# Kernel optimization log

Hardware: AMD Instinct MI355X
Metric: run time of the kernel (lower is better)

Reference implementation:

```python
import jax, jax.numpy as jnp
import numpy as np

T = 2048          # tokens (single causal sequence)
HID = 4096        # hidden_size
H = 32            # num_heads
DQ = 256          # per-head q/k dim (192 nope + 64 rope)
DN = 192          # nope dim
DR = 64           # rope dim
DV = 256          # v head dim
DKV = 512         # kv latent rank
QLORA = 2048      # q lora rank
EPS = 1e-6
THETA = 10000.0
SCALE = DQ ** -0.5


def rmsnorm(x, w):
    return x * jax.lax.rsqrt(jnp.mean(x * x, axis=-1, keepdims=True) + EPS) * w


def rope_neox(pos, x):
    # x: [T, h, DR]; neox style: rotate concatenated halves
    inv_freq = 1.0 / (THETA ** (jnp.arange(0, DR, 2, dtype=jnp.float32) / DR))  # [DR/2]
    ang = pos.astype(jnp.float32)[:, None] * inv_freq  # [T, DR/2]
    cos = jnp.cos(ang)[:, None, :]
    sin = jnp.sin(ang)[:, None, :]
    x1, x2 = jnp.split(x, 2, axis=-1)
    return jnp.concatenate([x1 * cos - x2 * sin, x2 * cos + x1 * sin], axis=-1)


def setup_inputs() -> dict:
    key = jax.random.key(0)
    ks = jax.random.split(key, 8)
    s = 0.02
    return {
        "hidden_states": jax.random.normal(ks[0], (T, HID), dtype=jnp.float32),
        "positions": jnp.arange(T, dtype=jnp.int32),
        "wq_a": jax.random.normal(ks[1], (HID, QLORA), dtype=jnp.float32) * s,
        "q_a_ln_w": jnp.ones((QLORA,), dtype=jnp.float32),
        "wq_b": jax.random.normal(ks[2], (QLORA, H * DQ), dtype=jnp.float32) * s,
        "wkv_a": jax.random.normal(ks[3], (HID, DKV + DR), dtype=jnp.float32) * s,
        "kv_a_ln_w": jnp.ones((DKV,), dtype=jnp.float32),
        "wkv_b": jax.random.normal(ks[4], (DKV, H * (DN + DV)), dtype=jnp.float32) * s,
        "wo": jax.random.normal(ks[5], (H * DV, HID), dtype=jnp.float32) * s,
    }


def reference(hidden_states, positions, wq_a, q_a_ln_w, wq_b, wkv_a, kv_a_ln_w, wkv_b, wo):
    # q path: lora down -> rmsnorm -> up -> [T, H, 256]
    q = rmsnorm(hidden_states @ wq_a, q_a_ln_w)
    q = (q @ wq_b).reshape(T, H, DQ)
    # kv path: latent 512 + shared k_pe 64
    latent = hidden_states @ wkv_a
    kv_a, k_pe = jnp.split(latent, [DKV], axis=-1)
    kv_a = rmsnorm(kv_a, kv_a_ln_w)
    kv = (kv_a @ wkv_b).reshape(T, H, DN + DV)
    k_nope, v = jnp.split(kv, [DN], axis=-1)
    q_nope, q_pe = jnp.split(q, [DN], axis=-1)
    k_pe = k_pe.reshape(T, 1, DR)
    q_pe = rope_neox(positions, q_pe)
    k_pe = rope_neox(positions, k_pe)
    q = jnp.concatenate([q_nope, q_pe], axis=-1)                       # [T, H, 256]
    k = jnp.concatenate([k_nope, jnp.broadcast_to(k_pe, (T, H, DR))], axis=-1)
    # causal attention
    scores = jnp.einsum("thd,shd->hts", q, k) * SCALE                  # [H, T, T]
    causal = jnp.tril(jnp.ones((T, T), dtype=bool))
    scores = jnp.where(causal[None], scores, jnp.finfo(scores.dtype).min)
    attn = jax.nn.softmax(scores, axis=-1)
    out = jnp.einsum("hts,shd->thd", attn, v).reshape(T, H * DV)
    return out @ wo
```

## Files before the change

### kernel.cpp

```cpp
#include <hip/hip_runtime.h>
#include <cstdint>
#include <cstddef>

#define T_    2048
#define HID_  4096
#define NH_   32
#define DQ_   256
#define DN_   192
#define DR_   64
#define DV_   256
#define DKV_  512
#define QL_   2048
#define NKV_  576
#define NKVP_ 640
#define HDQ_  8192
#define HDKV_ 14336
#define HDV_  8192
#define SCALE_ 0.0625f
#define MN5_  8388608
#define SK5_  2
#define MN1_  4194304
#define SK1_  4

using bf16x8 = __attribute__((ext_vector_type(8))) short;
using f32x4  = __attribute__((ext_vector_type(4))) float;

__device__ ushort g_hb   [(size_t)T_*HID_];
__device__ ushort g_wtqa [(size_t)QL_*HID_];
__device__ ushort g_wtqb [(size_t)HDQ_*QL_];
__device__ ushort g_wtkva[(size_t)NKVP_*HID_];
__device__ ushort g_wtkvb[(size_t)HDKV_*DKV_];
__device__ ushort g_wto  [(size_t)HID_*HDV_];
__device__ float  g_qa   [(size_t)T_*QL_];
__device__ ushort g_qn   [(size_t)T_*QL_];
__device__ ushort g_q    [(size_t)T_*HDQ_];
__device__ float  g_lat  [(size_t)T_*NKVP_];
__device__ ushort g_kvn  [(size_t)T_*DKV_];
__device__ ushort g_kpe  [(size_t)T_*DR_];
__device__ ushort g_kv   [(size_t)T_*HDKV_];
__device__ ushort g_k    [(size_t)NH_*T_*DQ_];
__device__ ushort g_vt   [(size_t)NH_*DV_*T_];
__device__ ushort g_o    [(size_t)T_*HDV_];
__device__ float  g_p5   [(size_t)SK5_*MN5_];

__device__ __forceinline__ float b2f(ushort h){ union{unsigned u; float f;} x; x.u=((unsigned)h)<<16; return x.f; }
__device__ __forceinline__ ushort f2b(float f){ union{float f; unsigned u;} x; x.f=f; unsigned r=x.u + 0x7fffu + ((x.u>>16)&1u); return (ushort)(r>>16); }
__device__ __forceinline__ void storeC(float*  p, float v){ *p = v; }
__device__ __forceinline__ void storeC(ushort* p, float v){ *p = f2b(v); }

#define GLD16(gp, lp) __builtin_amdgcn_global_load_lds( \
    (const __attribute__((address_space(1))) unsigned*)(gp), \
    (__attribute__((address_space(3))) unsigned*)(lp), 16, 0, 0)

__global__ __launch_bounds__(256) void convert_hidden(const float* __restrict__ src) {
  size_t i = ((size_t)blockIdx.x*256 + threadIdx.x)*4;
  float4 v = *(const float4*)(src + i);
  ushort4 o; o.x=f2b(v.x); o.y=f2b(v.y); o.z=f2b(v.z); o.w=f2b(v.w);
  *(ushort4*)(g_hb + i) = o;
}

__global__ __launch_bounds__(256) void transpose_w(const float* __restrict__ W,
                                                   ushort* __restrict__ Wt,
                                                   int K, int N, int Npad) {
  __shared__ float tile[64][33];
  const int bk = blockIdx.x*64, bn = blockIdx.y*32;
  const int tx = threadIdx.x & 31, ty = threadIdx.x >> 5;
  for (int r = ty; r < 64; r += 8) {
    int n = bn + tx;
    tile[r][tx] = (n < N) ? W[(size_t)(bk + r)*N + n] : 0.f;
  }
  __syncthreads();
  for (int rr = ty; rr < 32; rr += 8) {
    int n = bn + rr;
    unsigned pv = (unsigned)f2b(tile[2*tx][rr]) | ((unsigned)f2b(tile[2*tx+1][rr]) << 16);
    ((unsigned*)(Wt + (size_t)n*K))[(bk>>1) + tx] = pv;
  }
}

template<typename OutT>
__global__ __launch_bounds__(256) void gemm_bt(const ushort* __restrict__ A,
                                               const ushort* __restrict__ Bt,
                                               OutT* __restrict__ C,
                                               int M, int N, int K) {
  __shared__ ushort As[128*32];
  __shared__ ushort Bs[128*32];
  const int tid = threadIdx.x, lane = tid & 63, w = tid >> 6;
  const int wr = w >> 1, wc = w & 1, l15 = lane & 15, l4 = lane >> 4;
  const int m0 = blockIdx.x*128, n0 = blockIdx.y*128;
  f32x4 acc[4][4];
  #pragma unroll
  for (int i=0;i<4;i++)
    #pragma unroll
    for (int j=0;j<4;j++) acc[i][j] = f32x4{0.f,0.f,0.f,0.f};

  const int le0 = tid*8, le1 = (256+tid)*8;
  const int r0 = le0>>5, c0 = le0&31, r1 = le1>>5, c1 = le1&31;
  for (int k0 = 0; k0 < K; k0 += 32) {
    GLD16(A  + (size_t)(m0 + r0)*K + k0 + c0, ((ushort*)As)+le0);
    GLD16(A  + (size_t)(m0 + r1)*K + k0 + c1, ((ushort*)As)+le1);
    GLD16(Bt + (size_t)(n0 + r0)*K + k0 + c0, ((ushort*)Bs)+le0);
    GLD16(Bt + (size_t)(n0 + r1)*K + k0 + c1, ((ushort*)Bs)+le1);
    __syncthreads();
    bf16x8 af[4], bfr[4];
    #pragma unroll
    for (int i=0;i<4;i++) af[i]  = *(const bf16x8*)(As + (wr*64 + i*16 + l15)*32 + 8*l4);
    #pragma unroll
    for (int j=0;j<4;j++) bfr[j] = *(const bf16x8*)(Bs + (wc*64 + j*16 + l15)*32 + 8*l4);
    #pragma unroll
    for (int i=0;i<4;i++)
      #pragma unroll
      for (int j=0;j<4;j++)
        acc[i][j] = __builtin_amdgcn_mfma_f32_16x16x32_bf16(af[i], bfr[j], acc[i][j], 0,0,0);
    __syncthreads();
  }
  #pragma unroll
  for (int i=0;i<4;i++)
    #pragma unroll
    for (int j=0;j<4;j++) {
      const int row = m0 + wr*64 + i*16 + l4*4;
      const int col = n0 + wc*64 + j*16 + l15;
      #pragma unroll
      for (int r=0;r<4;r++) storeC(&C[(size_t)(row+r)*N + col], acc[i][j][r]);
    }
}

template<typename OutT, int S>
__global__ __launch_bounds__(512, 2) void gemm8(const ushort* __restrict__ A,
                                                const ushort* __restrict__ Bt,
                                                OutT* __restrict__ C,
                                                int M, int N, int Kfull, int pstride) {
  __shared__ ushort sm[65536];
  const int tid = threadIdx.x, lane = tid & 63, w = tid >> 6;
  const int wr = w >> 2, wc = w & 3, l15 = lane & 15, l4 = lane >> 4;
  const int swm = (l15 & 7) << 3;
  const int gm = M >> 8, gn = N >> 8;
  const int nb = gridDim.x, id = blockIdx.x;
  const int swz = (id & 7) * (nb >> 3) + (id >> 3);
  const int m0 = (swz % gm) << 8;
  const int rest = swz / gm;
  const int n0 = (rest % gn) << 8;
  const int ks = rest / gn;
  const int Ksl = Kfull / S;
  const int kofs = ks * Ksl;
  const int NT = Ksl >> 6;

#define STG_A(tt, qm) do { const int p_=(tt)&1, kb_=kofs+(tt)*64; \
    _Pragma("unroll") \
    for (int i_=0;i_<2;i_++){ \
      const int le_=(i_*512+tid)*8, r_=le_>>6, c_=le_&63; \
      const int tr_=(r_>>6)*128 + (qm)*64 + (r_&63); \
      GLD16(A + (size_t)(m0+tr_)*Kfull + kb_ + (c_ ^ ((r_&7)<<3)), \
            sm + p_*16384 + (qm)*8192 + le_); } } while(0)
#define STG_B(tt, qn) do { const int p_=(tt)&1, kb_=kofs+(tt)*64; \
    _Pragma("unroll") \
    for (int i_=0;i_<2;i_++){ \
      const int le_=(i_*512+tid)*8, r_=le_>>6, c_=le_&63; \
      const int tr_=(r_>>5)*64 + (qn)*32 + (r_&31); \
      GLD16(Bt + (size_t)(n0+tr_)*Kfull + kb_ + (c_ ^ ((r_&7)<<3)), \
            sm + 32768 + p_*16384 + (qn)*8192 + le_); } } while(0)

  f32x4 acc[8][4];
  #pragma unroll
  for (int i=0;i<8;i++)
    #pragma unroll
    for (int j=0;j<4;j++) acc[i][j] = f32x4{0.f,0.f,0.f,0.f};

  STG_A(0,0); STG_B(0,0); STG_A(0,1); STG_B(0,1);
  if (NT > 1) { STG_A(1,0); STG_B(1,0); }
  __builtin_amdgcn_sched_barrier(0);
  if (NT > 1) asm volatile("s_waitcnt vmcnt(4)" ::: "memory");
  else        asm volatile("s_waitcnt vmcnt(0)" ::: "memory");
  __builtin_amdgcn_sched_barrier(0);
  __builtin_amdgcn_s_barrier();

  for (int t = 0; t < NT; ++t) {
    const int p = t & 1;
    const ushort* Ab = sm + p*16384;
    const ushort* Bb = sm + 32768 + p*16384;
    bf16x8 af[4][2], bq0[2][2], bq1[2][2];

    #pragma unroll
    for (int mi=0;mi<4;mi++)
      #pragma unroll
      for (int k2=0;k2<2;k2++)
        af[mi][k2] = *(const bf16x8*)(Ab + (wr*64 + mi*16 + l15)*64 + ((k2*32 + 8*l4) ^ swm));
    #pragma unroll
    for (int nf=0;nf<2;nf++)
      #pragma unroll
      for (int k2=0;k2<2;k2++)
        bq0[nf][k2] = *(const bf16x8*)(Bb + (wc*32 + nf*16 + l15)*64 + ((k2*32 + 8*l4) ^ swm));
    if (t + 1 < NT) STG_A(t+1, 1);
    __builtin_amdgcn_sched_barrier(0);
    __builtin_amdgcn_s_barrier();
    __builtin_amdgcn_s_setprio(1);
    #pragma unroll
    for (int mi=0;mi<4;mi++)
      #pragma unroll
      for (int nf=0;nf<2;nf++)
        #pragma unroll
        for (int k2=0;k2<2;k2++)
          acc[mi][nf] = __builtin_amdgcn_mfma_f32_16x16x32_bf16(af[mi][k2], bq0[nf][k2], acc[mi][nf], 0,0,0);
    __builtin_amdgcn_s_setprio(0);
    __builtin_amdgcn_sched_barrier(0);
    __builtin_amdgcn_s_barrier();

    #pragma unroll
    for (int nf=0;nf<2;nf++)
      #pragma unroll
      for (int k2=0;k2<2;k2++)
        bq1[nf][k2] = *(const bf16x8*)(Bb + 8192 + (wc*32 + nf*16 + l15)*64 + ((k2*32 + 8*l4) ^ swm));
    if (t + 1 < NT) STG_B(t+1, 1);
    __builtin_amdgcn_sched_barrier(0);
    __builtin_amdgcn_s_barrier();
    __builtin_amdgcn_s_setprio(1);
    #pragma unroll
    for (int mi=0;mi<4;mi++)
      #pragma unroll
      for (int nf=0;nf<2;nf++)
        #pragma unroll
        for (int k2=0;k2<2;k2++)
          acc[mi][2+nf] = __builtin_amdgcn_mfma_f32_16x16x32_bf16(af[mi][k2], bq1[nf][k2], acc[mi][2+nf], 0,0,0);
    __builtin_amdgcn_s_setprio(0);
    __builtin_amdgcn_sched_barrier(0);
    __builtin_amdgcn_s_barrier();

    #pragma unroll
    for (int mi=0;mi<4;mi++)
      #pragma unroll
      for (int k2=0;k2<2;k2++)
        af[mi][k2] = *(const bf16x8*)(Ab + 8192 + (wr*64 + mi*16 + l15)*64 + ((k2*32 + 8*l4) ^ swm));
    if (t + 2 < NT) STG_A(t+2, 0);
    __builtin_amdgcn_sched_barrier(0);
    __builtin_amdgcn_s_barrier();
    __builtin_amdgcn_s_setprio(1);
    #pragma unroll
    for (int mi=0;mi<4;mi++)
      #pragma unroll
      for (int nf=0;nf<2;nf++)
        #pragma unroll
        for (int k2=0;k2<2;k2++)
          acc[4+mi][nf] = __builtin_amdgcn_mfma_f32_16x16x32_bf16(af[mi][k2], bq0[nf][k2], acc[4+mi][nf], 0,0,0);
    __builtin_amdgcn_s_setprio(0);
    __builtin_amdgcn_sched_barrier(0);
    __builtin_amdgcn_s_barrier();

    if (t + 2 < NT) STG_B(t+2, 0);
    __builtin_amdgcn_sched_barrier(0);
    if (t + 2 < NT)      asm volatile("s_waitcnt vmcnt(4)" ::: "memory");
    else if (t + 1 < NT) asm volatile("s_waitcnt vmcnt(0)" ::: "memory");
    __builtin_amdgcn_sched_barrier(0);
    __builtin_amdgcn_s_barrier();
    __builtin_amdgcn_s_setprio(1);
    #pragma unroll
    for (int mi=0;mi<4;mi++)
      #pragma unroll
      for (int nf=0;nf<2;nf++)
        #pragma unroll
        for (int k2=0;k2<2;k2++)
          acc[4+mi][2+nf] = __builtin_amdgcn_mfma_f32_16x16x32_bf16(af[mi][k2], bq1[nf][k2], acc[4+mi][2+nf], 0,0,0);
    __builtin_amdgcn_s_setprio(0);
    __builtin_amdgcn_sched_barrier(0);
    __builtin_amdgcn_s_barrier();
  }
#undef STG_A
#undef STG_B
  asm volatile("s_waitcnt vmcnt(0)" ::: "memory");

  #pragma unroll
  for (int mi=0;mi<8;mi++)
    #pragma unroll
    for (int nj=0;nj<4;nj++) {
      const int row = m0 + wr*128 + mi*16 + l4*4;
      const int col = n0 + wc*64 + nj*16 + l15;
      #pragma unroll
      for (int r=0;r<4;r++) {
        if (S == 1) storeC(&C[(size_t)(row+r)*N + col], acc[mi][nj][r]);
        else ((float*)C)[(size_t)ks*pstride + (size_t)(row+r)*N + col] = acc[mi][nj][r];
      }
    }
}

__global__ __launch_bounds__(256) void reduce5(const float* __restrict__ p, float* __restrict__ out) {
  size_t i = ((size_t)blockIdx.x*256 + threadIdx.x)*4;
  float4 a = *(const float4*)(p + i);
  #pragma unroll
  for (int s=1; s<SK5_; s++) {
    float4 b = *(const float4*)(p + (size_t)s*MN5_ + i);
    a.x+=b.x; a.y+=b.y; a.z+=b.z; a.w+=b.w;
  }
  *(float4*)(out + i) = a;
}

__global__ __launch_bounds__(256) void rmsnorm_q(const float* __restrict__ p,
                                                 const float* __restrict__ wln) {
  const int row = blockIdx.x;
  const float* x = p + (size_t)row*QL_;
  float* xo = g_qa + (size_t)row*QL_;
  float ss = 0.f;
  for (int i = threadIdx.x; i < QL_/4; i += 256) {
    float4 v = ((const float4*)x)[i];
    #pragma unroll
    for (int s=1; s<SK1_; s++) {
      float4 b = *(const float4*)(x + (size_t)s*MN1_ + i*4);
      v.x+=b.x; v.y+=b.y; v.z+=b.z; v.w+=b.w;
    }
    ((float4*)xo)[i] = v;
    ss += v.x*v.x + v.y*v.y + v.z*v.z + v.w*v.w;
  }
  #pragma unroll
  for (int o=32;o>=1;o>>=1) ss += __shfl_xor(ss, o);
  __shared__ float sr[4];
  if ((threadIdx.x & 63) == 0) sr[threadIdx.x>>6] = ss;
  __syncthreads();
  float rs = rsqrtf((sr[0]+sr[1]+sr[2]+sr[3])/(float)QL_ + 1e-6f);
  for (int i = threadIdx.x; i < QL_; i += 256)
    g_qn[(size_t)row*QL_ + i] = f2b(xo[i]*rs*wln[i]);
}

__global__ __launch_bounds__(256) void kv_norm_rope(const float* __restrict__ wln,
                                                    const int* __restrict__ pos) {
  const int t = blockIdx.x;
  const float* lat = g_lat + (size_t)t*NKVP_;
  float ss = 0.f;
  for (int i = threadIdx.x; i < DKV_; i += 256) ss += lat[i]*lat[i];
  #pragma unroll
  for (int o=32;o>=1;o>>=1) ss += __shfl_xor(ss, o);
  __shared__ float sr[4];
  if ((threadIdx.x & 63) == 0) sr[threadIdx.x>>6] = ss;
  __syncthreads();
  float rs = rsqrtf((sr[0]+sr[1]+sr[2]+sr[3])/(float)DKV_ + 1e-6f);
  for (int i = threadIdx.x; i < DKV_; i += 256)
    g_kvn[(size_t)t*DKV_ + i] = f2b(lat[i]*rs*wln[i]);
  if (threadIdx.x < 32) {
    const int i = threadIdx.x;
    float p = (float)pos[t];
    float ang = p * powf(10000.f, -(float)i/32.f);
    float c = cosf(ang), s = sinf(ang);
    float x1 = lat[DKV_ + i], x2 = lat[DKV_ + 32 + i];
    g_kpe[(size_t)t*DR_ + i]      = f2b(x1*c - x2*s);
    g_kpe[(size_t)t*DR_ + 32 + i] = f2b(x2*c + x1*s);
  }
}

__global__ __launch_bounds__(256) void q_rope(const int* __restrict__ pos) {
  const int t = blockIdx.x;
  __shared__ float cs[32], sn[32];
  if (threadIdx.x < 32) {
    const int i = threadIdx.x;
    float p = (float)pos[t];
    float ang = p * powf(10000.f, -(float)i/32.f);
    cs[i] = cosf(ang); sn[i] = sinf(ang);
  }
  __syncthreads();
  for (int e = threadIdx.x; e < NH_*32; e += 256) {
    const int h = e >> 5, i = e & 31;
    ushort* qp = g_q + (size_t)t*HDQ_ + h*DQ_ + DN_;
    float x1 = b2f(qp[i]), x2 = b2f(qp[32 + i]);
    qp[i]      = f2b(x1*cs[i] - x2*sn[i]);
    qp[32 + i] = f2b(x2*cs[i] + x1*sn[i]);
  }
}

__global__ __launch_bounds__(256) void build_k() {
  const int t = blockIdx.x;
  for (int e = threadIdx.x; e < NH_*32; e += 256) {
    const int h = e >> 5, d = (e & 31)*8;
    uint4 v;
    if (d < DN_) v = *(const uint4*)(g_kv  + (size_t)t*HDKV_ + h*448 + d);
    else         v = *(const uint4*)(g_kpe + (size_t)t*DR_ + (d - DN_));
    *(uint4*)(g_k + ((size_t)h*T_ + t)*DQ_ + d) = v;
  }
}

__global__ __launch_bounds__(256) void build_vt() {
  const int h = blockIdx.x, tt = blockIdx.y;
  __shared__ ushort tile[64*272];
  const int tid = threadIdx.x;
  #pragma unroll
  for (int p=0;p<8;p++) {
    int le = (p*256+tid)*8;
    int tl = le >> 8, d = le & 255;
    uint4 v = *(const uint4*)(g_kv + (size_t)(tt*64 + tl)*HDKV_ + h*448 + DN_ + d);
    *(uint4*)(tile + tl*272 + d) = v;
  }
  __syncthreads();
  #pragma unroll
  for (int p=0;p<8;p++) {
    int le = (p*256+tid)*8;
    int d = le >> 6, tl0 = le & 63;
    ushort tmp[8];
    #pragma unroll
    for (int j=0;j<8;j++) tmp[j] = tile[(tl0+j)*272 + d];
    *(uint4*)(g_vt + ((size_t)h*DV_ + d)*T_ + tt*64 + tl0) = *(const uint4*)tmp;
  }
}

__global__ __launch_bounds__(256) void attn_kernel() {
  __shared__ ushort KV[64*256];
  __shared__ ushort Pl[4][16][64];
  const int h = blockIdx.x;
  const int qt = (gridDim.y - 1) - blockIdx.y;
  const int tid = threadIdx.x, lane = tid & 63, w = tid >> 6;
  const int l15 = lane & 15, l4 = lane >> 4;
  const int swm = (l15 & 7) << 3;

  const ushort* Kh = g_k  + (size_t)h*T_*DQ_;
  const ushort* Vh = g_vt + (size_t)h*DV_*T_;

#define STAGE_K(kt_) do { \
    const ushort* ks_ = Kh + (size_t)(kt_)*64*DQ_; \
    _Pragma("unroll") \
    for (int c_=0;c_<8;c_++){ int le_=(c_*256+tid)*8, r_=le_>>8, co_=le_&255; \
      GLD16(ks_ + r_*256 + (co_ ^ ((r_&7)<<3)), KV+le_); } } while(0)
#define STAGE_V(kt_) do { \
    _Pragma("unroll") \
    for (int c_=0;c_<8;c_++){ int le_=(c_*256+tid)*8, d_=le_>>6, kv_=le_&63; \
      GLD16(Vh + (size_t)d_*T_ + (kt_)*64 + (kv_ ^ ((d_&7)<<3)), KV+le_); } } while(0)

  const int q0 = qt*64;
  const int qrow = q0 + w*16 + l15;

  bf16x8 qf[8];
  {
    const ushort* qb = g_q + (size_t)qrow*HDQ_ + h*DQ_;
    #pragma unroll
    for (int g=0; g<8; g++) qf[g] = *(const bf16x8*)(qb + 32*g + 8*l4);
  }
  f32x4 acc[16];
  #pragma unroll
  for (int i=0;i<16;i++) acc[i] = f32x4{0.f,0.f,0.f,0.f};
  float m_r = -1e30f, l_r = 0.f;

  STAGE_K(0);

  for (int kt = 0; kt <= qt; ++kt) {
    __builtin_amdgcn_sched_barrier(0);
    asm volatile("s_waitcnt vmcnt(0)" ::: "memory");
    __builtin_amdgcn_sched_barrier(0);
    __builtin_amdgcn_s_barrier();

    f32x4 s[4];
    #pragma unroll
    for (int fn=0; fn<4; fn++) s[fn] = f32x4{0.f,0.f,0.f,0.f};
    __builtin_amdgcn_s_setprio(1);
    #pragma unroll
    for (int g=0; g<8; g++)
      #pragma unroll
      for (int fn=0; fn<4; fn++) {
        bf16x8 kf = *(const bf16x8*)(KV + (fn*16 + l15)*256 + ((32*g + 8*l4) ^ swm));
        s[fn] = __builtin_amdgcn_mfma_f32_16x16x32_bf16(kf, qf[g], s[fn], 0,0,0);
      }
    __builtin_amdgcn_s_setprio(0);
    asm volatile("s_waitcnt lgkmcnt(0)" ::: "memory");
    __builtin_amdgcn_sched_barrier(0);
    __builtin_amdgcn_s_barrier();
    STAGE_V(kt);
    __builtin_amdgcn_sched_barrier(0);

    if (kt == qt) {
      #pragma unroll
      for (int fn=0; fn<4; fn++)
        #pragma unroll
        for (int r=0;r<4;r++) {
          int kv = kt*64 + fn*16 + l4*4 + r;
          if (kv > qrow) s[fn][r] = -1e30f;
        }
    }

    float mx = s[0][0];
    #pragma unroll
    for (int fn=0; fn<4; fn++)
      #pragma unroll
      for (int r=0;r<4;r++) mx = fmaxf(mx, s[fn][r]);
    mx = fmaxf(mx, __shfl_xor(mx, 16));
    mx = fmaxf(mx, __shfl_xor(mx, 32));
    mx *= SCALE_;
    if (__any(mx > m_r)) {
      float mn = fmaxf(m_r, mx);
      float sc = __expf(m_r - mn);
      m_r = mn;
      l_r *= sc;
      #pragma unroll
      for (int fd=0; fd<16; fd++)
        #pragma unroll
        for (int r=0;r<4;r++) acc[fd][r] *= sc;
    }
    float ssum = 0.f;
    #pragma unroll
    for (int fn=0; fn<4; fn++)
      #pragma unroll
      for (int r=0;r<4;r++) {
        float p = __expf(fmaf(s[fn][r], SCALE_, -m_r));
        s[fn][r] = p; ssum += p;
      }
    ssum += __shfl_xor(ssum, 16);
    ssum += __shfl_xor(ssum, 32);
    l_r += ssum;

    #pragma unroll
    for (int fn=0; fn<4; fn++) {
      ushort4 pw;
      pw.x = f2b(s[fn][0]); pw.y = f2b(s[fn][1]);
      pw.z = f2b(s[fn][2]); pw.w = f2b(s[fn][3]);
      *(ushort4*)(&Pl[w][l15][(fn*16 + l4*4) ^ swm]) = pw;
    }

    __builtin_amdgcn_sched_barrier(0);
    asm volatile("s_waitcnt vmcnt(0)" ::: "memory");
    __builtin_amdgcn_sched_barrier(0);
    __builtin_amdgcn_s_barrier();

    __builtin_amdgcn_s_setprio(1);
    #pragma unroll
    for (int s2=0; s2<2; s2++) {
      bf16x8 pa = *(const bf16x8*)(&Pl[w][l15][(s2*32 + 8*l4) ^ swm]);
      #pragma unroll
      for (int fd=0; fd<16; fd++) {
        bf16x8 vb = *(const bf16x8*)(KV + (fd*16 + l15)*64 + ((s2*32 + 8*l4) ^ swm));
        acc[fd] = __builtin_amdgcn_mfma_f32_16x16x32_bf16(vb, pa, acc[fd], 0,0,0);
      }
    }
    __builtin_amdgcn_s_setprio(0);
    asm volatile("s_waitcnt lgkmcnt(0)" ::: "memory");
    __builtin_amdgcn_sched_barrier(0);
    __builtin_amdgcn_s_barrier();
    if (kt < qt) STAGE_K(kt+1);
    __builtin_amdgcn_sched_barrier(0);
  }

  l_r = 1.f / l_r;
  #pragma unroll
  for (int fd=0; fd<16; fd++) {
    ushort4 ow;
    ow.x = f2b(acc[fd][0] * l_r); ow.y = f2b(acc[fd][1] * l_r);
    ow.z = f2b(acc[fd][2] * l_r); ow.w = f2b(acc[fd][3] * l_r);
    *(ushort4*)(g_o + (size_t)qrow*HDV_ + h*DV_ + fd*16 + l4*4) = ow;
  }
#undef STAGE_K
#undef STAGE_V
}

extern "C" void kernel_launch(void* const* d_in, const int* in_sizes, int n_in,
                              void* d_out, int out_size, void* d_ws, size_t ws_size,
                              hipStream_t stream) {
  (void)in_sizes; (void)n_in; (void)d_ws; (void)ws_size; (void)out_size;
  const float* hs    = (const float*)d_in[0];
  const int*   pos   = (const int*)  d_in[1];
  const float* wqa   = (const float*)d_in[2];
  const float* qlnw  = (const float*)d_in[3];
  const float* wqb   = (const float*)d_in[4];
  const float* wkva  = (const float*)d_in[5];
  const float* kvlnw = (const float*)d_in[6];
  const float* wkvb  = (const float*)d_in[7];
  const float* wo    = (const float*)d_in[8];
  float* out = (float*)d_out;

  void *p_hb, *p_wtqa, *p_wtqb, *p_wtkva, *p_wtkvb, *p_wto;
  void *p_qn, *p_q, *p_lat, *p_kvn, *p_kv, *p_o, *p_p5;
  hipGetSymbolAddress(&p_hb,    HIP_SYMBOL(g_hb));
  hipGetSymbolAddress(&p_wtqa,  HIP_SYMBOL(g_wtqa));
  hipGetSymbolAddress(&p_wtqb,  HIP_SYMBOL(g_wtqb));
  hipGetSymbolAddress(&p_wtkva, HIP_SYMBOL(g_wtkva));
  hipGetSymbolAddress(&p_wtkvb, HIP_SYMBOL(g_wtkvb));
  hipGetSymbolAddress(&p_wto,   HIP_SYMBOL(g_wto));
  hipGetSymbolAddress(&p_qn,    HIP_SYMBOL(g_qn));
  hipGetSymbolAddress(&p_q,     HIP_SYMBOL(g_q));
  hipGetSymbolAddress(&p_lat,   HIP_SYMBOL(g_lat));
  hipGetSymbolAddress(&p_kvn,   HIP_SYMBOL(g_kvn));
  hipGetSymbolAddress(&p_kv,    HIP_SYMBOL(g_kv));
  hipGetSymbolAddress(&p_o,    HIP_SYMBOL(g_o));
  hipGetSymbolAddress(&p_p5,    HIP_SYMBOL(g_p5));

  convert_hidden<<<8192, 256, 0, stream>>>(hs);
  transpose_w<<<dim3(HID_/64,  QL_/32),   256, 0, stream>>>(wqa,  (ushort*)p_wtqa,  HID_, QL_,   QL_);
  transpose_w<<<dim3(QL_/64,   HDQ_/32),  256, 0, stream>>>(wqb,  (ushort*)p_wtqb,  QL_,  HDQ_,  HDQ_);
  transpose_w<<<dim3(HID_/64,  NKVP_/32), 256, 0, stream>>>(wkva, (ushort*)p_wtkva, HID_, NKV_,  NKVP_);
  transpose_w<<<dim3(DKV_/64,  HDKV_/32), 256, 0, stream>>>(wkvb, (ushort*)p_wtkvb, DKV_, HDKV_, HDKV_);
  transpose_w<<<dim3(HDV_/64,  HID_/32),  256, 0, stream>>>(wo,   (ushort*)p_wto,   HDV_, HID_,  HID_);

  gemm8<float,SK1_><<<(T_/256)*(QL_/256)*SK1_, 512, 0, stream>>>((const ushort*)p_hb, (const ushort*)p_wtqa, (float*)p_p5, T_, QL_, HID_, MN1_);
  rmsnorm_q<<<T_, 256, 0, stream>>>((const float*)p_p5, qlnw);
  gemm8<ushort,1><<<(T_/256)*(HDQ_/256), 512, 0, stream>>>((const ushort*)p_qn, (const ushort*)p_wtqb, (ushort*)p_q, T_, HDQ_, QL_, 0);

  gemm_bt<float ><<<dim3(T_/128, NKVP_/128), 256, 0, stream>>>((const ushort*)p_hb, (const ushort*)p_wtkva, (float*)p_lat, T_, NKVP_, HID_);
  kv_norm_rope<<<T_, 256, 0, stream>>>(kvlnw, pos);
  q_rope<<<T_, 256, 0, stream>>>(pos);
  gemm8<ushort,1><<<(T_/256)*(HDKV_/256), 512, 0, stream>>>((const ushort*)p_kvn, (const ushort*)p_wtkvb, (ushort*)p_kv, T_, HDKV_, DKV_, 0);

  build_k<<<T_, 256, 0, stream>>>();
  build_vt<<<dim3(NH_, T_/64), 256, 0, stream>>>();
  attn_kernel<<<dim3(NH_, 32), 256, 0, stream>>>();

  gemm8<float,SK5_><<<(T_/256)*(HID_/256)*SK5_, 512, 0, stream>>>((const ushort*)p_o, (const ushort*)p_wto, (float*)p_p5, T_, HID_, HDV_, MN5_);
  reduce5<<<MN5_/1024, 256, 0, stream>>>((const float*)p_p5, out);
}
```

Before: 836.3 us.

## Fuse q_a and kv_a down-projections into one concatenated split-K GEMM

Concatenates the transposed wq_a and wkv_a weights into one 2816-wide B matrix so both down-projections from hidden_states run in a single gemm8 launch with split-K of 4. This drops the slower 128-tile gemm_bt kernel and lets the kv path use the tuned 256-tile kernel while reading A only once. kv_norm_rope now sums the split-K partials itself into shared memory. The cost is extra partial-sum traffic for the kv columns and a larger partial buffer. 2816 is 11×256, so the extra kv columns (2048..2815, with 576 real and the rest zero-padded) fit the tiles exactly.

```diff
diff --git a/kernel.cpp b/kernel.cpp
--- a/kernel.cpp
+++ b/kernel.cpp
@@ -12,36 +12,34 @@
 #define DKV_  512
 #define QL_   2048
 #define NKV_  576
-#define NKVP_ 640
 #define HDQ_  8192
 #define HDKV_ 14336
 #define HDV_  8192
 #define SCALE_ 0.0625f
 #define MN5_  8388608
 #define SK5_  2
-#define MN1_  4194304
+#define NKC_  2816
+#define PS1_  5767168
 #define SK1_  4
 
 using bf16x8 = __attribute__((ext_vector_type(8))) short;
 using f32x4  = __attribute__((ext_vector_type(4))) float;
 
 __device__ ushort g_hb   [(size_t)T_*HID_];
-__device__ ushort g_wtqa [(size_t)QL_*HID_];
+__device__ ushort g_wtc  [(size_t)NKC_*HID_];
 __device__ ushort g_wtqb [(size_t)HDQ_*QL_];
-__device__ ushort g_wtkva[(size_t)NKVP_*HID_];
 __device__ ushort g_wtkvb[(size_t)HDKV_*DKV_];
 __device__ ushort g_wto  [(size_t)HID_*HDV_];
 __device__ float  g_qa   [(size_t)T_*QL_];
 __device__ ushort g_qn   [(size_t)T_*QL_];
 __device__ ushort g_q    [(size_t)T_*HDQ_];
-__device__ float  g_lat  [(size_t)T_*NKVP_];
 __device__ ushort g_kvn  [(size_t)T_*DKV_];
 __device__ ushort g_kpe  [(size_t)T_*DR_];
 __device__ ushort g_kv   [(size_t)T_*HDKV_];
 __device__ ushort g_k    [(size_t)NH_*T_*DQ_];
 __device__ ushort g_vt   [(size_t)NH_*DV_*T_];
 __device__ ushort g_o    [(size_t)T_*HDV_];
-__device__ float  g_p5   [(size_t)SK5_*MN5_];
+__device__ float  g_p5   [(size_t)SK1_*PS1_];
 
 __device__ __forceinline__ float b2f(ushort h){ union{unsigned u; float f;} x; x.u=((unsigned)h)<<16; return x.f; }
 __device__ __forceinline__ ushort f2b(float f){ union{float f; unsigned u;} x; x.f=f; unsigned r=x.u + 0x7fffu + ((x.u>>16)&1u); return (ushort)(r>>16); }
@@ -61,7 +59,7 @@
 
 __global__ __launch_bounds__(256) void transpose_w(const float* __restrict__ W,
                                                    ushort* __restrict__ Wt,
-                                                   int K, int N, int Npad) {
+                                                   int K, int N) {
   __shared__ float tile[64][33];
   const int bk = blockIdx.x*64, bn = blockIdx.y*32;
   const int tx = threadIdx.x & 31, ty = threadIdx.x >> 5;
@@ -75,53 +73,6 @@
     unsigned pv = (unsigned)f2b(tile[2*tx][rr]) | ((unsigned)f2b(tile[2*tx+1][rr]) << 16);
     ((unsigned*)(Wt + (size_t)n*K))[(bk>>1) + tx] = pv;
   }
-}
-
-template<typename OutT>
-__global__ __launch_bounds__(256) void gemm_bt(const ushort* __restrict__ A,
-                                               const ushort* __restrict__ Bt,
-                                               OutT* __restrict__ C,
-                                               int M, int N, int K) {
-  __shared__ ushort As[128*32];
-  __shared__ ushort Bs[128*32];
-  const int tid = threadIdx.x, lane = tid & 63, w = tid >> 6;
-  const int wr = w >> 1, wc = w & 1, l15 = lane & 15, l4 = lane >> 4;
-  const int m0 = blockIdx.x*128, n0 = blockIdx.y*128;
-  f32x4 acc[4][4];
-  #pragma unroll
-  for (int i=0;i<4;i++)
-    #pragma unroll
-    for (int j=0;j<4;j++) acc[i][j] = f32x4{0.f,0.f,0.f,0.f};
-
-  const int le0 = tid*8, le1 = (256+tid)*8;
-  const int r0 = le0>>5, c0 = le0&31, r1 = le1>>5, c1 = le1&31;
-  for (int k0 = 0; k0 < K; k0 += 32) {
-    GLD16(A  + (size_t)(m0 + r0)*K + k0 + c0, ((ushort*)As)+le0);
-    GLD16(A  + (size_t)(m0 + r1)*K + k0 + c1, ((ushort*)As)+le1);
-    GLD16(Bt + (size_t)(n0 + r0)*K + k0 + c0, ((ushort*)Bs)+le0);
-    GLD16(Bt + (size_t)(n0 + r1)*K + k0 + c1, ((ushort*)Bs)+le1);
-    __syncthreads();
-    bf16x8 af[4], bfr[4];
-    #pragma unroll
-    for (int i=0;i<4;i++) af[i]  = *(const bf16x8*)(As + (wr*64 + i*16 + l15)*32 + 8*l4);
-    #pragma unroll
-    for (int j=0;j<4;j++) bfr[j] = *(const bf16x8*)(Bs + (wc*64 + j*16 + l15)*32 + 8*l4);
-    #pragma unroll
-    for (int i=0;i<4;i++)
-      #pragma unroll
-      for (int j=0;j<4;j++)
-        acc[i][j] = __builtin_amdgcn_mfma_f32_16x16x32_bf16(af[i], bfr[j], acc[i][j], 0,0,0);
-    __syncthreads();
-  }
-  #pragma unroll
-  for (int i=0;i<4;i++)
-    #pragma unroll
-    for (int j=0;j<4;j++) {
-      const int row = m0 + wr*64 + i*16 + l4*4;
-      const int col = n0 + wc*64 + j*16 + l15;
-      #pragma unroll
-      for (int r=0;r<4;r++) storeC(&C[(size_t)(row+r)*N + col], acc[i][j][r]);
-    }
 }
 
 template<typename OutT, int S>
@@ -294,14 +245,14 @@
 __global__ __launch_bounds__(256) void rmsnorm_q(const float* __restrict__ p,
                                                  const float* __restrict__ wln) {
   const int row = blockIdx.x;
-  const float* x = p + (size_t)row*QL_;
+  const float* x = p + (size_t)row*NKC_;
   float* xo = g_qa + (size_t)row*QL_;
   float ss = 0.f;
   for (int i = threadIdx.x; i < QL_/4; i += 256) {
-    float4 v = ((const float4*)x)[i];
+    float4 v = *(const float4*)(x + i*4);
     #pragma unroll
     for (int s=1; s<SK1_; s++) {
-      float4 b = *(const float4*)(x + (size_t)s*MN1_ + i*4);
+      float4 b = *(const float4*)(x + (size_t)s*PS1_ + i*4);
       v.x+=b.x; v.y+=b.y; v.z+=b.z; v.w+=b.w;
     }
     ((float4*)xo)[i] = v;
@@ -317,12 +268,20 @@
     g_qn[(size_t)row*QL_ + i] = f2b(xo[i]*rs*wln[i]);
 }
 
-__global__ __launch_bounds__(256) void kv_norm_rope(const float* __restrict__ wln,
+__global__ __launch_bounds__(256) void kv_norm_rope(const float* __restrict__ p,
+                                                    const float* __restrict__ wln,
                                                     const int* __restrict__ pos) {
   const int t = blockIdx.x;
-  const float* lat = g_lat + (size_t)t*NKVP_;
+  const float* base = p + (size_t)t*NKC_ + QL_;
+  __shared__ float lat[NKV_];
   float ss = 0.f;
-  for (int i = threadIdx.x; i < DKV_; i += 256) ss += lat[i]*lat[i];
+  for (int i = threadIdx.x; i < NKV_; i += 256) {
+    float v = base[i];
+    #pragma unroll
+    for (int s=1; s<SK1_; s++) v += base[(size_t)s*PS1_ + i];
+    lat[i] = v;
+    if (i < DKV_) ss += v*v;
+  }
   #pragma unroll
   for (int o=32;o>=1;o>>=1) ss += __shfl_xor(ss, o);
   __shared__ float sr[4];
@@ -333,8 +292,8 @@
     g_kvn[(size_t)t*DKV_ + i] = f2b(lat[i]*rs*wln[i]);
   if (threadIdx.x < 32) {
     const int i = threadIdx.x;
-    float p = (float)pos[t];
-    float ang = p * powf(10000.f, -(float)i/32.f);
+    float pp = (float)pos[t];
+    float ang = pp * powf(10000.f, -(float)i/32.f);
     float c = cosf(ang), s = sinf(ang);
     float x1 = lat[DKV_ + i], x2 = lat[DKV_ + 32 + i];
     g_kpe[(size_t)t*DR_ + i]      = f2b(x1*c - x2*s);
@@ -555,35 +514,32 @@
   const float* wo    = (const float*)d_in[8];
   float* out = (float*)d_out;
 
-  void *p_hb, *p_wtqa, *p_wtqb, *p_wtkva, *p_wtkvb, *p_wto;
-  void *p_qn, *p_q, *p_lat, *p_kvn, *p_kv, *p_o, *p_p5;
+  void *p_hb, *p_wtc, *p_wtqb, *p_wtkvb, *p_wto;
+  void *p_qn, *p_q, *p_kvn, *p_kv, *p_o, *p_p5;
   hipGetSymbolAddress(&p_hb,    HIP_SYMBOL(g_hb));
-  hipGetSymbolAddress(&p_wtqa,  HIP_SYMBOL(g_wtqa));
+  hipGetSymbolAddress(&p_wtc,   HIP_SYMBOL(g_wtc));
   hipGetSymbolAddress(&p_wtqb,  HIP_SYMBOL(g_wtqb));
-  hipGetSymbolAddress(&p_wtkva, HIP_SYMBOL(g_wtkva));
   hipGetSymbolAddress(&p_wtkvb, HIP_SYMBOL(g_wtkvb));
   hipGetSymbolAddress(&p_wto,   HIP_SYMBOL(g_wto));
   hipGetSymbolAddress(&p_qn,    HIP_SYMBOL(g_qn));
   hipGetSymbolAddress(&p_q,     HIP_SYMBOL(g_q));
-  hipGetSymbolAddress(&p_lat,   HIP_SYMBOL(g_lat));
   hipGetSymbolAddress(&p_kvn,   HIP_SYMBOL(g_kvn));
   hipGetSymbolAddress(&p_kv,    HIP_SYMBOL(g_kv));
-  hipGetSymbolAddress(&p_o,    HIP_SYMBOL(g_o));
+  hipGetSymbolAddress(&p_o,     HIP_SYMBOL(g_o));
   hipGetSymbolAddress(&p_p5,    HIP_SYMBOL(g_p5));
 
   convert_hidden<<<8192, 256, 0, stream>>>(hs);
-  transpose_w<<<dim3(HID_/64,  QL_/32),   256, 0, stream>>>(wqa,  (ushort*)p_wtqa,  HID_, QL_,   QL_);
-  transpose_w<<<dim3(QL_/64,   HDQ_/32),  256, 0, stream>>>(wqb,  (ushort*)p_wtqb,  QL_,  HDQ_,  HDQ_);
-  transpose_w<<<dim3(HID_/64,  NKVP_/32), 256, 0, stream>>>(wkva, (ushort*)p_wtkva, HID_, NKV_,  NKVP_);
-  transpose_w<<<dim3(DKV_/64,  HDKV_/32), 256, 0, stream>>>(wkvb, (ushort*)p_wtkvb, DKV_, HDKV_, HDKV_);
-  transpose_w<<<dim3(HDV_/64,  HID_/32),  256, 0, stream>>>(wo,   (ushort*)p_wto,   HDV_, HID_,  HID_);
-
-  gemm8<float,SK1_><<<(T_/256)*(QL_/256)*SK1_, 512, 0, stream>>>((const ushort*)p_hb, (const ushort*)p_wtqa, (float*)p_p5, T_, QL_, HID_, MN1_);
+  transpose_w<<<dim3(HID_/64,  QL_/32),        256, 0, stream>>>(wqa,  (ushort*)p_wtc,                        HID_, QL_);
+  transpose_w<<<dim3(HID_/64, (NKC_-QL_)/32),  256, 0, stream>>>(wkva, (ushort*)p_wtc + (size_t)QL_*HID_,     HID_, NKV_);
+  transpose_w<<<dim3(QL_/64,   HDQ_/32),       256, 0, stream>>>(wqb,  (ushort*)p_wtqb,  QL_,  HDQ_);
+  transpose_w<<<dim3(DKV_/64,  HDKV_/32),      256, 0, stream>>>(wkvb, (ushort*)p_wtkvb, DKV_, HDKV_);
+  transpose_w<<<dim3(HDV_/64,  HID_/32),       256, 0, stream>>>(wo,   (ushort*)p_wto,   HDV_, HID_);
+
+  gemm8<float,SK1_><<<(T_/256)*(NKC_/256)*SK1_, 512, 0, stream>>>((const ushort*)p_hb, (const ushort*)p_wtc, (float*)p_p5, T_, NKC_, HID_, PS1_);
   rmsnorm_q<<<T_, 256, 0, stream>>>((const float*)p_p5, qlnw);
+  kv_norm_rope<<<T_, 256, 0, stream>>>((const float*)p_p5, kvlnw, pos);
+
   gemm8<ushort,1><<<(T_/256)*(HDQ_/256), 512, 0, stream>>>((const ushort*)p_qn, (const ushort*)p_wtqb, (ushort*)p_q, T_, HDQ_, QL_, 0);
-
-  gemm_bt<float ><<<dim3(T_/128, NKVP_/128), 256, 0, stream>>>((const ushort*)p_hb, (const ushort*)p_wtkva, (float*)p_lat, T_, NKVP_, HID_);
-  kv_norm_rope<<<T_, 256, 0, stream>>>(kvlnw, pos);
   q_rope<<<T_, 256, 0, stream>>>(pos);
   gemm8<ushort,1><<<(T_/256)*(HDKV_/256), 512, 0, stream>>>((const ushort*)p_kvn, (const ushort*)p_wtkvb, (ushort*)p_kv, T_, HDKV_, DKV_, 0);
 
```

Result: faster. 756.1 us (-9.6%).
